# Kernel tuning notes

Hardware: AMD Instinct MI355X
Metric: run time of the kernel (lower is better)

## Reference

```python
import jax, jax.numpy as jnp
import numpy as np
from jax import lax

LN_EPS = 1e-6  # flax LayerNorm default


def _layernorm(x, scale, bias):
    mu = jnp.mean(x, axis=-1, keepdims=True)
    var = jnp.mean(jnp.square(x - mu), axis=-1, keepdims=True)
    return (x - mu) * lax.rsqrt(var + LN_EPS) * scale + bias


def _lstm_layer(c0, h0, Wi, Wh, b, x):
    # x: [B, T, F]; carry c/h: [B, H]; gate order i, f, g, o (flax)
    def step(carry, xt):
        c, h = carry
        z = xt @ Wi + h @ Wh + b  # [B, 4H]
        i, f, g, o = jnp.split(z, 4, axis=-1)
        i = jax.nn.sigmoid(i); f = jax.nn.sigmoid(f)
        g = jnp.tanh(g); o = jax.nn.sigmoid(o)
        c = f * c + i * g
        h = o * jnp.tanh(c)
        return (c, h), h
    (cT, hT), hs = lax.scan(step, (c0, h0), jnp.swapaxes(x, 0, 1))
    return cT, hT, jnp.swapaxes(hs, 0, 1)  # hs: [B, T, H]


def setup_inputs() -> dict:
    key = jax.random.key(0)
    ks = jax.random.split(key, 16)
    B, T, F, H, P, A = 64, 128, 512, 1024, 1024, 32
    s = 0.05
    return {
        "x": jax.random.normal(ks[0], (B, T, F), jnp.float32),
        "c0": jnp.zeros((2, B, H), jnp.float32),
        "h0": jnp.zeros((2, B, H), jnp.float32),
        "W_pre": jax.random.normal(ks[1], (F, P), jnp.float32) * s,
        "b_pre": jnp.zeros((P,), jnp.float32),
        "ln_scale": jnp.ones((P,), jnp.float32),
        "ln_bias": jnp.zeros((P,), jnp.float32),
        "Wi0": jax.random.normal(ks[2], (P, 4 * H), jnp.float32) * s,
        "Wh0": jax.random.normal(ks[3], (H, 4 * H), jnp.float32) * s,
        "b0": jnp.zeros((4 * H,), jnp.float32),
        "Wi1": jax.random.normal(ks[4], (H, 4 * H), jnp.float32) * s,
        "Wh1": jax.random.normal(ks[5], (H, 4 * H), jnp.float32) * s,
        "b1": jnp.zeros((4 * H,), jnp.float32),
        "W_post": jax.random.normal(ks[6], (H, P), jnp.float32) * s,
        "b_post": jnp.zeros((P,), jnp.float32),
        "W_out": jax.random.normal(ks[7], (P, A), jnp.float32) * s,
        "b_out": jnp.zeros((A,), jnp.float32),
        "training": False,
    }


def reference(x, c0, h0, W_pre, b_pre, ln_scale, ln_bias,
              Wi0, Wh0, b0, Wi1, Wh1, b1,
              W_post, b_post, W_out, b_out, training):
    # preprocessing: Dense -> LayerNorm -> relu
    h = jax.nn.relu(_layernorm(x @ W_pre + b_pre, ln_scale, ln_bias))
    # two stacked LSTM layers scanned over time
    c1, h1, h = _lstm_layer(c0[0], h0[0], Wi0, Wh0, b0, h)
    c2, h2, h = _lstm_layer(c0[1], h0[1], Wi1, Wh1, b1, h)
    # postprocessing: Dense -> relu (dropout deterministic => identity)
    h = jax.nn.relu(h @ W_post + b_post)
    logits = h @ W_out + b_out  # [B, T, action_dim]
    new_carry = (jnp.stack([c1, c2]), jnp.stack([h1, h2]))
    return new_carry, logits
```

## Files before the change

### kernel.cpp

```cpp
#include <hip/hip_runtime.h>
#include <hip/hip_bf16.h>
#include <math.h>

typedef __attribute__((ext_vector_type(8))) short short8;
typedef __attribute__((ext_vector_type(4))) float f32x4;
typedef __attribute__((ext_vector_type(4))) unsigned u32x4;
typedef unsigned short u16;
typedef unsigned long long u64;

__device__ __forceinline__ u16 f2bf(float f) {
    union { float f; unsigned u; } v; v.f = f;
    unsigned r = v.u + 0x7fffu + ((v.u >> 16) & 1u);
    return (u16)(r >> 16);
}
__device__ __forceinline__ float bf2f(u16 b) {
    union { unsigned u; float f; } v; v.u = ((unsigned)b) << 16;
    return v.f;
}
__device__ __forceinline__ float fast_sigmoid(float x) {
    return __builtin_amdgcn_rcpf(1.f + __expf(-x));
}
__device__ __forceinline__ float fast_tanh(float x) {
    return 1.f - 2.f * __builtin_amdgcn_rcpf(1.f + __expf(2.f * x));
}
__device__ __forceinline__ u32x4 ldg16(const void* p) {
    u32x4 r;
    asm volatile("global_load_dwordx4 %0, %1, off"
                 : "=v"(r) : "v"(p) : "memory");
    return r;
}


__global__ __launch_bounds__(256) void k_zero(unsigned* p, int n) {
    int i = blockIdx.x * 256 + threadIdx.x;
    if (i < n) p[i] = 0u;
}

__global__ __launch_bounds__(256) void k_cvt(const float* __restrict__ in,
                                             u16* __restrict__ out, int n) {
    int i = blockIdx.x * 256 + threadIdx.x;
    if (i < n) out[i] = f2bf(in[i]);
}

__global__ __launch_bounds__(256) void k_cvt_h(const float* __restrict__ in,
                                               u16* __restrict__ out) {
    int i = blockIdx.x * 256 + threadIdx.x;
    int b = i >> 10, j = i & 1023;
    out[(size_t)(j >> 3) * 512 + b * 8 + (j & 7)] = f2bf(in[i]);
}

__global__ __launch_bounds__(256) void k_transpose(const float* __restrict__ W,
                                                   u16* __restrict__ WT, int K, int N) {
    __shared__ float tile[32][33];
    int n0 = blockIdx.x * 32, k0 = blockIdx.y * 32;
    int tx = threadIdx.x & 31, ty = threadIdx.x >> 5;
    #pragma unroll
    for (int j = 0; j < 32; j += 8)
        tile[ty + j][tx] = W[(size_t)(k0 + ty + j) * N + n0 + tx];
    __syncthreads();
    #pragma unroll
    for (int j = 0; j < 32; j += 8)
        WT[(size_t)(n0 + ty + j) * K + k0 + tx] = f2bf(tile[tx][ty + j]);
}

template <int MODE>
__global__ __launch_bounds__(256) void k_gemm(const u16* __restrict__ A,
                                              const u16* __restrict__ BT,
                                              const float* __restrict__ bias,
                                              void* __restrict__ Cout,
                                              int M, int N, int K) {
    const int w = threadIdx.x >> 6, l = threadIdx.x & 63;
    const int lm = l & 15, lq = l >> 4;
    const int r0 = blockIdx.y * 64 + w * 16;
    const int c0 = blockIdx.x * 64;
    const u16* arow = A + (size_t)(r0 + lm) * K + lq * 8;
    const u16* bp0 = BT + (size_t)(c0 + lm) * K + lq * 8;
    const u16* bp1 = bp0 + (size_t)16 * K;
    const u16* bp2 = bp0 + (size_t)32 * K;
    const u16* bp3 = bp0 + (size_t)48 * K;
    f32x4 acc0 = {0.f, 0.f, 0.f, 0.f}, acc1 = acc0, acc2 = acc0, acc3 = acc0;
    for (int k0 = 0; k0 < K; k0 += 32) {
        short8 a = *(const short8*)(arow + k0);
        acc0 = __builtin_amdgcn_mfma_f32_16x16x32_bf16(a, *(const short8*)(bp0 + k0), acc0, 0, 0, 0);
        acc1 = __builtin_amdgcn_mfma_f32_16x16x32_bf16(a, *(const short8*)(bp1 + k0), acc1, 0, 0, 0);
        acc2 = __builtin_amdgcn_mfma_f32_16x16x32_bf16(a, *(const short8*)(bp2 + k0), acc2, 0, 0, 0);
        acc3 = __builtin_amdgcn_mfma_f32_16x16x32_bf16(a, *(const short8*)(bp3 + k0), acc3, 0, 0, 0);
    }
    f32x4 accs[4] = {acc0, acc1, acc2, acc3};
    #pragma unroll
    for (int nt = 0; nt < 4; nt++) {
        #pragma unroll
        for (int r = 0; r < 4; r++) {
            int row = r0 + lq * 4 + r;
            int col = c0 + nt * 16 + lm;
            float v = accs[nt][r] + bias[col];
            if (MODE == 0) {
                ((float*)Cout)[(size_t)row * N + col] = v;
            } else {
                if (MODE == 2) v = fmaxf(v, 0.f);
                ((u16*)Cout)[(size_t)row * N + col] = f2bf(v);
            }
        }
    }
}

__global__ __launch_bounds__(256) void k_ln_relu(const float* __restrict__ X,
                                                 const float* __restrict__ scale,
                                                 const float* __restrict__ bias,
                                                 u16* __restrict__ preS) {
    const int N = 1024;
    int row = blockIdx.x;
    int b = row >> 7, t = row & 127;
    const float* x = X + (size_t)row * N;
    __shared__ float vbuf[1024];
    float s = 0.f, ss = 0.f;
    float vals[4];
    #pragma unroll
    for (int j = 0; j < 4; j++) {
        float v = x[threadIdx.x + 256 * j];
        vals[j] = v; s += v; ss += v * v;
    }
    #pragma unroll
    for (int o = 32; o > 0; o >>= 1) { s += __shfl_down(s, o); ss += __shfl_down(ss, o); }
    __shared__ float rs[4], rss[4];
    int w = threadIdx.x >> 6;
    if ((threadIdx.x & 63) == 0) { rs[w] = s; rss[w] = ss; }
    __syncthreads();
    __shared__ float smu, sinv;
    if (threadIdx.x == 0) {
        float a = rs[0] + rs[1] + rs[2] + rs[3];
        float bq = rss[0] + rss[1] + rss[2] + rss[3];
        float mu = a * (1.f / N);
        float var = bq * (1.f / N) - mu * mu;
        smu = mu; sinv = rsqrtf(var + 1e-6f);
    }
    __syncthreads();
    float mu = smu, inv = sinv;
    #pragma unroll
    for (int j = 0; j < 4; j++) {
        int i = threadIdx.x + 256 * j;
        float v = (vals[j] - mu) * inv * scale[i] + bias[i];
        vbuf[i] = fmaxf(v, 0.f);
    }
    __syncthreads();
    if (threadIdx.x < 128) {
        int g = threadIdx.x;
        union { u16 h[8]; u32x4 v; } pk;
        #pragma unroll
        for (int e = 0; e < 8; e++) pk.h[e] = f2bf(vbuf[g * 8 + e]);
        *(u32x4*)(preS + (size_t)t * 65536 + (size_t)g * 512 + b * 8) = pk.v;
    }
}

#define FBLOCKS 256
__global__ __launch_bounds__(512, 1) void k_lstm_fused(
    const u16* __restrict__ WiT0, const u16* __restrict__ WhT0,
    const u16* __restrict__ WiT1, const u16* __restrict__ WhT1,
    const u16* __restrict__ preS, const float* __restrict__ b0v,
    const float* __restrict__ b1v, const float* __restrict__ c0_all,
    u16* __restrict__ hs0, u16* __restrict__ hs1, u16* __restrict__ Hp,
    float* __restrict__ out, unsigned* __restrict__ ctr) {
    const int bk = blockIdx.x;
    const int role = bk >> 7;
    const int bkl = bk & 127;
    const int tid = threadIdx.x;
    const int w = tid >> 6, l = tid & 63, lm = l & 15, lq = l >> 4;
    const int kp = w >> 2, rt = w & 3;

    __shared__ u16 whs[65536];
    __shared__ float zbuf[2 * 64 * 33];
    __shared__ int gflag[2];

    {
        const u16* Wx = role ? WiT1 : WiT0;
        const u16* Wh = role ? WhT1 : WhT0;
        for (int f = tid; f < 8192; f += 512) {
            int flm = f & 15, flq = (f >> 4) & 3;
            int fi = (f >> 6) & 31;
            int rest = f >> 11;
            int fg = rest & 1, fkp = (rest >> 1) & 1;
            int lc = fg * 16 + flm;
            int gcolw = (lc >> 3) * 1024 + bkl * 8 + (lc & 7);
            int k = fi * 32 + flq * 8;
            const u16* src = (fkp == 0 ? Wx : Wh) + (size_t)gcolw * 1024 + k;
            *(short8*)(whs + (size_t)f * 8) = *(const short8*)src;
        }
    }
    if (tid == 0) { gflag[0] = -1; gflag[1] = -1; }
    const int u = tid & 7, b = tid >> 3;
    const int gcol = bkl * 8 + u;
    float c = (c0_all + (size_t)role * 65536)[(size_t)b * 1024 + gcol];
    const float* bv = role ? b1v : b0v;
    float bi0 = bv[gcol], bi1 = bv[1024 + gcol];
    float bi2 = bv[2048 + gcol], bi3 = bv[3072 + gcol];
    u16* hs_my = role ? hs1 : hs0;
    float* c_out = out + (size_t)role * 65536;
    float* h_out = out + 131072 + (size_t)role * 65536;
    const int lanoff = (lq * 16 + lm) * 8;
    __syncthreads();

    for (int t = 0; t < 128; t++) {
        if (role || kp == 1) {
            int need = (role && kp == 0) ? t + 1 : t;
            if (rt == 0) {
                if (need > 0) {
                    int cbase = (role && kp) ? 128 : 0;
                    for (;;) {
                        unsigned a0 = __hip_atomic_load(&ctr[(cbase + l) * 16], __ATOMIC_RELAXED,
                                                        __HIP_MEMORY_SCOPE_AGENT);
                        unsigned a1 = __hip_atomic_load(&ctr[(cbase + 64 + l) * 16], __ATOMIC_RELAXED,
                                                        __HIP_MEMORY_SCOPE_AGENT);
                        if (__all((a0 >= (unsigned)need) && (a1 >= (unsigned)need))) break;
                        __builtin_amdgcn_s_sleep(1);
                    }
                }
                __hip_atomic_store(&gflag[kp], need, __ATOMIC_RELAXED,
                                   __HIP_MEMORY_SCOPE_WORKGROUP);
            } else {
                while (__hip_atomic_load(&gflag[kp], __ATOMIC_RELAXED,
                                         __HIP_MEMORY_SCOPE_WORKGROUP) < need)
                    __builtin_amdgcn_s_sleep(1);
            }
        }

        const u16* abase;
        if (!role) abase = (kp == 0) ? preS + (size_t)t * 65536
                                     : hs0 + (size_t)t * 65536;
        else       abase = (kp == 0) ? hs0 + (size_t)(t + 1) * 65536
                                     : hs1 + (size_t)t * 65536;
        const u16* arow = abase + (size_t)lq * 512 + (rt * 16 + lm) * 8;
        const u16* bw0 = whs + kp * 32768 + lanoff;

        f32x4 acc0 = {0.f, 0.f, 0.f, 0.f}, acc1 = acc0;
        #define STEPF(Ai, i)                                                      \
        {   union { u32x4 q; short8 v; } _a; _a.q = (Ai);                         \
            short8 _b0 = *(const short8*)(bw0 + (i) * 512);                       \
            short8 _b1 = *(const short8*)(bw0 + 16384 + (i) * 512);               \
            acc0 = __builtin_amdgcn_mfma_f32_16x16x32_bf16(_a.v, _b0, acc0, 0, 0, 0); \
            acc1 = __builtin_amdgcn_mfma_f32_16x16x32_bf16(_a.v, _b1, acc1, 0, 0, 0); }

        u32x4 A0 = ldg16(arow +     0), A1 = ldg16(arow +  2048);
        u32x4 A2 = ldg16(arow +  4096), A3 = ldg16(arow +  6144);
        u32x4 A4 = ldg16(arow +  8192), A5 = ldg16(arow + 10240);
        u32x4 A6 = ldg16(arow + 12288), A7 = ldg16(arow + 14336);
        u32x4 A8 = ldg16(arow + 16384), A9 = ldg16(arow + 18432);
        u32x4 A10 = ldg16(arow + 20480), A11 = ldg16(arow + 22528);
        u32x4 A12 = ldg16(arow + 24576), A13 = ldg16(arow + 26624);
        u32x4 A14 = ldg16(arow + 28672), A15 = ldg16(arow + 30720);
        u32x4 A16 = ldg16(arow + 32768), A17 = ldg16(arow + 34816);
        u32x4 A18 = ldg16(arow + 36864), A19 = ldg16(arow + 38912);
        u32x4 A20 = ldg16(arow + 40960), A21 = ldg16(arow + 43008);
        u32x4 A22 = ldg16(arow + 45056), A23 = ldg16(arow + 47104);
        u32x4 A24 = ldg16(arow + 49152), A25 = ldg16(arow + 51200);
        u32x4 A26 = ldg16(arow + 53248), A27 = ldg16(arow + 55296);
        u32x4 A28 = ldg16(arow + 57344), A29 = ldg16(arow + 59392);
        u32x4 A30 = ldg16(arow + 61440), A31 = ldg16(arow + 63488);
        asm volatile("s_waitcnt vmcnt(24)"
                     : "+v"(A0), "+v"(A1), "+v"(A2), "+v"(A3),
                       "+v"(A4), "+v"(A5), "+v"(A6), "+v"(A7) :: "memory");
        STEPF(A0, 0) STEPF(A1, 1) STEPF(A2, 2) STEPF(A3, 3)
        STEPF(A4, 4) STEPF(A5, 5) STEPF(A6, 6) STEPF(A7, 7)
        asm volatile("s_waitcnt vmcnt(16)"
                     : "+v"(A8), "+v"(A9), "+v"(A10), "+v"(A11),
                       "+v"(A12), "+v"(A13), "+v"(A14), "+v"(A15) :: "memory");
        STEPF(A8, 8) STEPF(A9, 9) STEPF(A10, 10) STEPF(A11, 11)
        STEPF(A12, 12) STEPF(A13, 13) STEPF(A14, 14) STEPF(A15, 15)
        asm volatile("s_waitcnt vmcnt(8)"
                     : "+v"(A16), "+v"(A17), "+v"(A18), "+v"(A19),
                       "+v"(A20), "+v"(A21), "+v"(A22), "+v"(A23) :: "memory");
        STEPF(A16, 16) STEPF(A17, 17) STEPF(A18, 18) STEPF(A19, 19)
        STEPF(A20, 20) STEPF(A21, 21) STEPF(A22, 22) STEPF(A23, 23)
        asm volatile("s_waitcnt vmcnt(0)"
                     : "+v"(A24), "+v"(A25), "+v"(A26), "+v"(A27),
                       "+v"(A28), "+v"(A29), "+v"(A30), "+v"(A31) :: "memory");
        STEPF(A24, 24) STEPF(A25, 25) STEPF(A26, 26) STEPF(A27, 27)
        STEPF(A28, 28) STEPF(A29, 29) STEPF(A30, 30) STEPF(A31, 31)
        #undef STEPF

        {
            float* zb = zbuf + (size_t)kp * 2112;
            #pragma unroll
            for (int r = 0; r < 4; r++) {
                int row = rt * 16 + lq * 4 + r;
                zb[row * 33 + lm] = acc0[r];
                zb[row * 33 + 16 + lm] = acc1[r];
            }
        }
        __syncthreads();

        {
            const float* z0 = zbuf + (size_t)b * 33;
            const float* z1 = z0 + 2112;
            float gi = z0[u]      + z1[u]      + bi0;
            float gf = z0[8 + u]  + z1[8 + u]  + bi1;
            float gg = z0[16 + u] + z1[16 + u] + bi2;
            float go = z0[24 + u] + z1[24 + u] + bi3;
            gi = fast_sigmoid(gi);
            gf = fast_sigmoid(gf);
            gg = fast_tanh(gg);
            go = fast_sigmoid(go);
            c = gf * c + gi * gg;
            float h = go * fast_tanh(c);
            unsigned hv = (unsigned)f2bf(h);
            int base = l & 56;
            unsigned p0 = __shfl(hv, base + 0, 64) | (__shfl(hv, base + 1, 64) << 16);
            unsigned p1 = __shfl(hv, base + 2, 64) | (__shfl(hv, base + 3, 64) << 16);
            unsigned p2 = __shfl(hv, base + 4, 64) | (__shfl(hv, base + 5, 64) << 16);
            unsigned p3 = __shfl(hv, base + 6, 64) | (__shfl(hv, base + 7, 64) << 16);
            if (u == 0) {
                u32x4 pv = {p0, p1, p2, p3};
                u16* dst = hs_my + (size_t)(t + 1) * 65536 + (size_t)bkl * 512 + b * 8;
                asm volatile("global_store_dwordx4 %0, %1, off sc0 sc1"
                             :: "v"(dst), "v"(pv) : "memory");
                if (role) {
                    u16* d2 = Hp + (size_t)(t * 64 + b) * 1024 + bkl * 8;
                    *(u32x4*)d2 = pv;
                }
            }
            if (t == 127) {
                c_out[(size_t)b * 1024 + gcol] = c;
                h_out[(size_t)b * 1024 + gcol] = h;
            }
        }
        __syncthreads();

        if (tid == 0)
            __hip_atomic_store(&ctr[bk * 16], (unsigned)(t + 1), __ATOMIC_RELAXED,
                               __HIP_MEMORY_SCOPE_AGENT);
    }
}

__global__ __launch_bounds__(256) void k_logits(const u16* __restrict__ Pact,
                                                const u16* __restrict__ WoT,
                                                const float* __restrict__ bout,
                                                float* __restrict__ out) {
    int r = blockIdx.x * 8 + (threadIdx.x >> 5);
    int n = threadIdx.x & 31;
    const u16* a = Pact + (size_t)r * 1024;
    const u16* wv = WoT + (size_t)n * 1024;
    float s = 0.f;
    for (int k = 0; k < 1024; k += 8) {
        short8 av = *(const short8*)(a + k);
        short8 wvv = *(const short8*)(wv + k);
        #pragma unroll
        for (int j = 0; j < 8; j++)
            s += bf2f((u16)av[j]) * bf2f((u16)wvv[j]);
    }
    int t = r >> 6, b = r & 63;
    out[((size_t)b * 128 + t) * 32 + n] = s + bout[n];
}

extern "C" void kernel_launch(void* const* d_in, const int* in_sizes, int n_in,
                              void* d_out, int out_size, void* d_ws, size_t ws_size,
                              hipStream_t stream) {
    const float* x      = (const float*)d_in[0];
    const float* c0     = (const float*)d_in[1];
    const float* h0     = (const float*)d_in[2];
    const float* W_pre  = (const float*)d_in[3];
    const float* b_pre  = (const float*)d_in[4];
    const float* ln_s   = (const float*)d_in[5];
    const float* ln_b   = (const float*)d_in[6];
    const float* Wi0    = (const float*)d_in[7];
    const float* Wh0    = (const float*)d_in[8];
    const float* b0     = (const float*)d_in[9];
    const float* Wi1    = (const float*)d_in[10];
    const float* Wh1    = (const float*)d_in[11];
    const float* b1     = (const float*)d_in[12];
    const float* W_post = (const float*)d_in[13];
    const float* b_post = (const float*)d_in[14];
    const float* W_out  = (const float*)d_in[15];
    const float* b_out  = (const float*)d_in[16];
    float* out = (float*)d_out;

    char* ws = (char*)d_ws;
    size_t off = 0;
    auto alloc = [&](size_t bytes) {
        void* p = ws + off;
        off += (bytes + 255) & ~(size_t)255;
        return p;
    };
    u16* WTpre  = (u16*)alloc((size_t)1024 * 512 * 2);
    u16* WTi0   = (u16*)alloc((size_t)4096 * 1024 * 2);
    u16* WTh0   = (u16*)alloc((size_t)4096 * 1024 * 2);
    u16* WTi1   = (u16*)alloc((size_t)4096 * 1024 * 2);
    u16* WTh1   = (u16*)alloc((size_t)4096 * 1024 * 2);
    u16* WTpost = (u16*)alloc((size_t)1024 * 1024 * 2);
    u16* WTout  = (u16*)alloc((size_t)32 * 1024 * 2);
    u16* Xb     = (u16*)alloc((size_t)8192 * 512 * 2);
    u16* preS   = (u16*)alloc((size_t)128 * 65536 * 2);
    u16* hs0    = (u16*)alloc((size_t)129 * 65536 * 2);
    u16* hs1    = (u16*)alloc((size_t)129 * 65536 * 2);
    u16* postact= (u16*)alloc((size_t)8192 * 1024 * 2);
    unsigned* ctr = (unsigned*)alloc(32768);
    void* unionreg = alloc((size_t)8192 * 4096 * 2);
    float* pre_f32 = (float*)unionreg;
    u16* Hplain = (u16*)unionreg;

    k_zero<<<32, 256, 0, stream>>>(ctr, 8192);
    k_cvt<<<(8192 * 512) / 256, 256, 0, stream>>>(x, Xb, 8192 * 512);
    k_cvt_h<<<256, 256, 0, stream>>>(h0, hs0);
    k_cvt_h<<<256, 256, 0, stream>>>(h0 + 65536, hs1);

    k_transpose<<<dim3(32, 16), 256, 0, stream>>>(W_pre, WTpre, 512, 1024);
    k_transpose<<<dim3(128, 32), 256, 0, stream>>>(Wi0, WTi0, 1024, 4096);
    k_transpose<<<dim3(128, 32), 256, 0, stream>>>(Wh0, WTh0, 1024, 4096);
    k_transpose<<<dim3(128, 32), 256, 0, stream>>>(Wi1, WTi1, 1024, 4096);
    k_transpose<<<dim3(128, 32), 256, 0, stream>>>(Wh1, WTh1, 1024, 4096);
    k_transpose<<<dim3(32, 32), 256, 0, stream>>>(W_post, WTpost, 1024, 1024);
    k_transpose<<<dim3(1, 32), 256, 0, stream>>>(W_out, WTout, 1024, 32);

    k_gemm<0><<<dim3(16, 128), 256, 0, stream>>>(Xb, WTpre, b_pre, pre_f32, 8192, 1024, 512);
    k_ln_relu<<<8192, 256, 0, stream>>>(pre_f32, ln_s, ln_b, preS);

    {
        const u16* WiT0_ = WTi0; const u16* WhT0_ = WTh0;
        const u16* WiT1_ = WTi1; const u16* WhT1_ = WTh1;
        const u16* preS_ = preS; const float* b0_ = b0; const float* b1_ = b1;
        const float* c0_ = c0; u16* hs0_ = hs0; u16* hs1_ = hs1;
        u16* Hp_ = Hplain; float* out_ = out; unsigned* ctr_ = ctr;
        void* args[] = {&WiT0_, &WhT0_, &WiT1_, &WhT1_, &preS_, &b0_, &b1_,
                        &c0_, &hs0_, &hs1_, &Hp_, &out_, &ctr_};
        hipLaunchCooperativeKernel((void*)k_lstm_fused, dim3(FBLOCKS), dim3(512),
                                   args, 0, stream);
    }

    k_gemm<2><<<dim3(16, 128), 256, 0, stream>>>(Hplain, WTpost, b_post, postact,
                                                 8192, 1024, 1024);
    k_logits<<<1024, 256, 0, stream>>>(postact, WTout, b_out, out + 262144);
}
```

Baseline: 1.154 ms.

## Replace layer-0 recurrent counter barrier with sentinel-polled data readiness

For the layer-0 recurrent half, the per-step wait on global atomic counters from all 128 blocks is replaced by polling the hidden-state data itself. A shadow buffer is pre-filled with a NaN bf16 sentinel, each block writes its new h there, and readers spin until the loaded values no longer match the sentinel. This lets each wave start its MFMA groups as soon as its own slice arrives, removing a counter round-trip and the workgroup flag handoff. The cost is an extra store per step, a fill kernel, and extra cache-bypassing reloads. It also assumes a real hidden value can never equal the sentinel pattern.

```diff
diff --git a/kernel.cpp b/kernel.cpp
--- a/kernel.cpp
+++ b/kernel.cpp
@@ -29,11 +29,23 @@
                  : "=v"(r) : "v"(p) : "memory");
     return r;
 }
+__device__ __forceinline__ u32x4 ldg16sc(const void* p) {
+    u32x4 r;
+    asm volatile("global_load_dwordx4 %0, %1, off sc0 sc1"
+                 : "=v"(r) : "v"(p) : "memory");
+    return r;
+}
 
 
 __global__ __launch_bounds__(256) void k_zero(unsigned* p, int n) {
     int i = blockIdx.x * 256 + threadIdx.x;
     if (i < n) p[i] = 0u;
+}
+
+__global__ __launch_bounds__(256) void k_fill_sent(u32x4* p, int n) {
+    int i = blockIdx.x * 256 + threadIdx.x;
+    u32x4 s = {0x7F807F80u, 0x7F807F80u, 0x7F807F80u, 0x7F807F80u};
+    if (i < n) p[i] = s;
 }
 
 __global__ __launch_bounds__(256) void k_cvt(const float* __restrict__ in,
@@ -158,8 +170,8 @@
     const u16* __restrict__ WiT1, const u16* __restrict__ WhT1,
     const u16* __restrict__ preS, const float* __restrict__ b0v,
     const float* __restrict__ b1v, const float* __restrict__ c0_all,
-    u16* __restrict__ hs0, u16* __restrict__ hs1, u16* __restrict__ Hp,
-    float* __restrict__ out, unsigned* __restrict__ ctr) {
+    u16* __restrict__ hs0, u16* __restrict__ hs1, u16* __restrict__ hsS,
+    u16* __restrict__ Hp, float* __restrict__ out, unsigned* __restrict__ ctr) {
     const int bk = blockIdx.x;
     const int role = bk >> 7;
     const int bkl = bk & 127;
@@ -200,38 +212,9 @@
     __syncthreads();
 
     for (int t = 0; t < 128; t++) {
-        if (role || kp == 1) {
-            int need = (role && kp == 0) ? t + 1 : t;
-            if (rt == 0) {
-                if (need > 0) {
-                    int cbase = (role && kp) ? 128 : 0;
-                    for (;;) {
-                        unsigned a0 = __hip_atomic_load(&ctr[(cbase + l) * 16], __ATOMIC_RELAXED,
-                                                        __HIP_MEMORY_SCOPE_AGENT);
-                        unsigned a1 = __hip_atomic_load(&ctr[(cbase + 64 + l) * 16], __ATOMIC_RELAXED,
-                                                        __HIP_MEMORY_SCOPE_AGENT);
-                        if (__all((a0 >= (unsigned)need) && (a1 >= (unsigned)need))) break;
-                        __builtin_amdgcn_s_sleep(1);
-                    }
-                }
-                __hip_atomic_store(&gflag[kp], need, __ATOMIC_RELAXED,
-                                   __HIP_MEMORY_SCOPE_WORKGROUP);
-            } else {
-                while (__hip_atomic_load(&gflag[kp], __ATOMIC_RELAXED,
-                                         __HIP_MEMORY_SCOPE_WORKGROUP) < need)
-                    __builtin_amdgcn_s_sleep(1);
-            }
-        }
-
-        const u16* abase;
-        if (!role) abase = (kp == 0) ? preS + (size_t)t * 65536
-                                     : hs0 + (size_t)t * 65536;
-        else       abase = (kp == 0) ? hs0 + (size_t)(t + 1) * 65536
-                                     : hs1 + (size_t)t * 65536;
-        const u16* arow = abase + (size_t)lq * 512 + (rt * 16 + lm) * 8;
         const u16* bw0 = whs + kp * 32768 + lanoff;
-
         f32x4 acc0 = {0.f, 0.f, 0.f, 0.f}, acc1 = acc0;
+
         #define STEPF(Ai, i)                                                      \
         {   union { u32x4 q; short8 v; } _a; _a.q = (Ai);                         \
             short8 _b0 = *(const short8*)(bw0 + (i) * 512);                       \
@@ -239,42 +222,134 @@
             acc0 = __builtin_amdgcn_mfma_f32_16x16x32_bf16(_a.v, _b0, acc0, 0, 0, 0); \
             acc1 = __builtin_amdgcn_mfma_f32_16x16x32_bf16(_a.v, _b1, acc1, 0, 0, 0); }
 
-        u32x4 A0 = ldg16(arow +     0), A1 = ldg16(arow +  2048);
-        u32x4 A2 = ldg16(arow +  4096), A3 = ldg16(arow +  6144);
-        u32x4 A4 = ldg16(arow +  8192), A5 = ldg16(arow + 10240);
-        u32x4 A6 = ldg16(arow + 12288), A7 = ldg16(arow + 14336);
-        u32x4 A8 = ldg16(arow + 16384), A9 = ldg16(arow + 18432);
-        u32x4 A10 = ldg16(arow + 20480), A11 = ldg16(arow + 22528);
-        u32x4 A12 = ldg16(arow + 24576), A13 = ldg16(arow + 26624);
-        u32x4 A14 = ldg16(arow + 28672), A15 = ldg16(arow + 30720);
-        u32x4 A16 = ldg16(arow + 32768), A17 = ldg16(arow + 34816);
-        u32x4 A18 = ldg16(arow + 36864), A19 = ldg16(arow + 38912);
-        u32x4 A20 = ldg16(arow + 40960), A21 = ldg16(arow + 43008);
-        u32x4 A22 = ldg16(arow + 45056), A23 = ldg16(arow + 47104);
-        u32x4 A24 = ldg16(arow + 49152), A25 = ldg16(arow + 51200);
-        u32x4 A26 = ldg16(arow + 53248), A27 = ldg16(arow + 55296);
-        u32x4 A28 = ldg16(arow + 57344), A29 = ldg16(arow + 59392);
-        u32x4 A30 = ldg16(arow + 61440), A31 = ldg16(arow + 63488);
-        asm volatile("s_waitcnt vmcnt(24)"
-                     : "+v"(A0), "+v"(A1), "+v"(A2), "+v"(A3),
-                       "+v"(A4), "+v"(A5), "+v"(A6), "+v"(A7) :: "memory");
-        STEPF(A0, 0) STEPF(A1, 1) STEPF(A2, 2) STEPF(A3, 3)
-        STEPF(A4, 4) STEPF(A5, 5) STEPF(A6, 6) STEPF(A7, 7)
-        asm volatile("s_waitcnt vmcnt(16)"
-                     : "+v"(A8), "+v"(A9), "+v"(A10), "+v"(A11),
-                       "+v"(A12), "+v"(A13), "+v"(A14), "+v"(A15) :: "memory");
-        STEPF(A8, 8) STEPF(A9, 9) STEPF(A10, 10) STEPF(A11, 11)
-        STEPF(A12, 12) STEPF(A13, 13) STEPF(A14, 14) STEPF(A15, 15)
-        asm volatile("s_waitcnt vmcnt(8)"
-                     : "+v"(A16), "+v"(A17), "+v"(A18), "+v"(A19),
-                       "+v"(A20), "+v"(A21), "+v"(A22), "+v"(A23) :: "memory");
-        STEPF(A16, 16) STEPF(A17, 17) STEPF(A18, 18) STEPF(A19, 19)
-        STEPF(A20, 20) STEPF(A21, 21) STEPF(A22, 22) STEPF(A23, 23)
-        asm volatile("s_waitcnt vmcnt(0)"
-                     : "+v"(A24), "+v"(A25), "+v"(A26), "+v"(A27),
-                       "+v"(A28), "+v"(A29), "+v"(A30), "+v"(A31) :: "memory");
-        STEPF(A24, 24) STEPF(A25, 25) STEPF(A26, 26) STEPF(A27, 27)
-        STEPF(A28, 28) STEPF(A29, 29) STEPF(A30, 30) STEPF(A31, 31)
+        if (!role && kp == 1) {
+            const u16* arow = hsS + (size_t)t * 65536 + lq * 512 + (rt * 16 + lm) * 8;
+            #define CHK4(q) (((q)[0] != 0x7F807F80u) && ((q)[1] != 0x7F807F80u) && \
+                             ((q)[2] != 0x7F807F80u) && ((q)[3] != 0x7F807F80u))
+            #define SGROUP(B0,B1,B2,B3,B4,B5,B6,B7,o0,o1,o2,o3,o4,o5,o6,o7)       \
+            for (;;) {                                                            \
+                int _ok = CHK4(B0) && CHK4(B1) && CHK4(B2) && CHK4(B3) &&         \
+                          CHK4(B4) && CHK4(B5) && CHK4(B6) && CHK4(B7);           \
+                if (__all(_ok)) break;                                            \
+                B0 = ldg16sc(arow + o0); B1 = ldg16sc(arow + o1);                 \
+                B2 = ldg16sc(arow + o2); B3 = ldg16sc(arow + o3);                 \
+                B4 = ldg16sc(arow + o4); B5 = ldg16sc(arow + o5);                 \
+                B6 = ldg16sc(arow + o6); B7 = ldg16sc(arow + o7);                 \
+                asm volatile("s_waitcnt vmcnt(0)"                                 \
+                             : "+v"(B0), "+v"(B1), "+v"(B2), "+v"(B3),            \
+                               "+v"(B4), "+v"(B5), "+v"(B6), "+v"(B7) :: "memory"); \
+            }
+            u32x4 A0 = ldg16sc(arow +     0), A1 = ldg16sc(arow +  2048);
+            u32x4 A2 = ldg16sc(arow +  4096), A3 = ldg16sc(arow +  6144);
+            u32x4 A4 = ldg16sc(arow +  8192), A5 = ldg16sc(arow + 10240);
+            u32x4 A6 = ldg16sc(arow + 12288), A7 = ldg16sc(arow + 14336);
+            u32x4 A8 = ldg16sc(arow + 16384), A9 = ldg16sc(arow + 18432);
+            u32x4 A10 = ldg16sc(arow + 20480), A11 = ldg16sc(arow + 22528);
+            u32x4 A12 = ldg16sc(arow + 24576), A13 = ldg16sc(arow + 26624);
+            u32x4 A14 = ldg16sc(arow + 28672), A15 = ldg16sc(arow + 30720);
+            u32x4 A16 = ldg16sc(arow + 32768), A17 = ldg16sc(arow + 34816);
+            u32x4 A18 = ldg16sc(arow + 36864), A19 = ldg16sc(arow + 38912);
+            u32x4 A20 = ldg16sc(arow + 40960), A21 = ldg16sc(arow + 43008);
+            u32x4 A22 = ldg16sc(arow + 45056), A23 = ldg16sc(arow + 47104);
+            u32x4 A24 = ldg16sc(arow + 49152), A25 = ldg16sc(arow + 51200);
+            u32x4 A26 = ldg16sc(arow + 53248), A27 = ldg16sc(arow + 55296);
+            u32x4 A28 = ldg16sc(arow + 57344), A29 = ldg16sc(arow + 59392);
+            u32x4 A30 = ldg16sc(arow + 61440), A31 = ldg16sc(arow + 63488);
+            asm volatile("s_waitcnt vmcnt(24)"
+                         : "+v"(A0), "+v"(A1), "+v"(A2), "+v"(A3),
+                           "+v"(A4), "+v"(A5), "+v"(A6), "+v"(A7) :: "memory");
+            SGROUP(A0,A1,A2,A3,A4,A5,A6,A7, 0,2048,4096,6144,8192,10240,12288,14336)
+            STEPF(A0, 0) STEPF(A1, 1) STEPF(A2, 2) STEPF(A3, 3)
+            STEPF(A4, 4) STEPF(A5, 5) STEPF(A6, 6) STEPF(A7, 7)
+            asm volatile("s_waitcnt vmcnt(16)"
+                         : "+v"(A8), "+v"(A9), "+v"(A10), "+v"(A11),
+                           "+v"(A12), "+v"(A13), "+v"(A14), "+v"(A15) :: "memory");
+            SGROUP(A8,A9,A10,A11,A12,A13,A14,A15,
+                   16384,18432,20480,22528,24576,26624,28672,30720)
+            STEPF(A8, 8) STEPF(A9, 9) STEPF(A10, 10) STEPF(A11, 11)
+            STEPF(A12, 12) STEPF(A13, 13) STEPF(A14, 14) STEPF(A15, 15)
+            asm volatile("s_waitcnt vmcnt(8)"
+                         : "+v"(A16), "+v"(A17), "+v"(A18), "+v"(A19),
+                           "+v"(A20), "+v"(A21), "+v"(A22), "+v"(A23) :: "memory");
+            SGROUP(A16,A17,A18,A19,A20,A21,A22,A23,
+                   32768,34816,36864,38912,40960,43008,45056,47104)
+            STEPF(A16, 16) STEPF(A17, 17) STEPF(A18, 18) STEPF(A19, 19)
+            STEPF(A20, 20) STEPF(A21, 21) STEPF(A22, 22) STEPF(A23, 23)
+            asm volatile("s_waitcnt vmcnt(0)"
+                         : "+v"(A24), "+v"(A25), "+v"(A26), "+v"(A27),
+                           "+v"(A28), "+v"(A29), "+v"(A30), "+v"(A31) :: "memory");
+            SGROUP(A24,A25,A26,A27,A28,A29,A30,A31,
+                   49152,51200,53248,55296,57344,59392,61440,63488)
+            STEPF(A24, 24) STEPF(A25, 25) STEPF(A26, 26) STEPF(A27, 27)
+            STEPF(A28, 28) STEPF(A29, 29) STEPF(A30, 30) STEPF(A31, 31)
+            #undef SGROUP
+            #undef CHK4
+        } else {
+            if (role) {
+                int need = (kp == 0) ? t + 1 : t;
+                if (rt == 0) {
+                    if (need > 0) {
+                        int cbase = kp ? 128 : 0;
+                        for (;;) {
+                            unsigned a0 = __hip_atomic_load(&ctr[(cbase + l) * 16], __ATOMIC_RELAXED,
+                                                            __HIP_MEMORY_SCOPE_AGENT);
+                            unsigned a1 = __hip_atomic_load(&ctr[(cbase + 64 + l) * 16], __ATOMIC_RELAXED,
+                                                            __HIP_MEMORY_SCOPE_AGENT);
+                            if (__all((a0 >= (unsigned)need) && (a1 >= (unsigned)need))) break;
+                            __builtin_amdgcn_s_sleep(1);
+                        }
+                    }
+                    __hip_atomic_store(&gflag[kp], need, __ATOMIC_RELAXED,
+                                       __HIP_MEMORY_SCOPE_WORKGROUP);
+                } else {
+                    while (__hip_atomic_load(&gflag[kp], __ATOMIC_RELAXED,
+                                             __HIP_MEMORY_SCOPE_WORKGROUP) < need)
+                        __builtin_amdgcn_s_sleep(1);
+                }
+            }
+            const u16* abase;
+            if (!role) abase = preS + (size_t)t * 65536;
+            else       abase = (kp == 0) ? hs0 + (size_t)(t + 1) * 65536
+                                         : hs1 + (size_t)t * 65536;
+            const u16* arow = abase + (size_t)lq * 512 + (rt * 16 + lm) * 8;
+
+            u32x4 A0 = ldg16(arow +     0), A1 = ldg16(arow +  2048);
+            u32x4 A2 = ldg16(arow +  4096), A3 = ldg16(arow +  6144);
+            u32x4 A4 = ldg16(arow +  8192), A5 = ldg16(arow + 10240);
+            u32x4 A6 = ldg16(arow + 12288), A7 = ldg16(arow + 14336);
+            u32x4 A8 = ldg16(arow + 16384), A9 = ldg16(arow + 18432);
+            u32x4 A10 = ldg16(arow + 20480), A11 = ldg16(arow + 22528);
+            u32x4 A12 = ldg16(arow + 24576), A13 = ldg16(arow + 26624);
+            u32x4 A14 = ldg16(arow + 28672), A15 = ldg16(arow + 30720);
+            u32x4 A16 = ldg16(arow + 32768), A17 = ldg16(arow + 34816);
+            u32x4 A18 = ldg16(arow + 36864), A19 = ldg16(arow + 38912);
+            u32x4 A20 = ldg16(arow + 40960), A21 = ldg16(arow + 43008);
+            u32x4 A22 = ldg16(arow + 45056), A23 = ldg16(arow + 47104);
+            u32x4 A24 = ldg16(arow + 49152), A25 = ldg16(arow + 51200);
+            u32x4 A26 = ldg16(arow + 53248), A27 = ldg16(arow + 55296);
+            u32x4 A28 = ldg16(arow + 57344), A29 = ldg16(arow + 59392);
+            u32x4 A30 = ldg16(arow + 61440), A31 = ldg16(arow + 63488);
+            asm volatile("s_waitcnt vmcnt(24)"
+                         : "+v"(A0), "+v"(A1), "+v"(A2), "+v"(A3),
+                           "+v"(A4), "+v"(A5), "+v"(A6), "+v"(A7) :: "memory");
+            STEPF(A0, 0) STEPF(A1, 1) STEPF(A2, 2) STEPF(A3, 3)
+            STEPF(A4, 4) STEPF(A5, 5) STEPF(A6, 6) STEPF(A7, 7)
+            asm volatile("s_waitcnt vmcnt(16)"
+                         : "+v"(A8), "+v"(A9), "+v"(A10), "+v"(A11),
+                           "+v"(A12), "+v"(A13), "+v"(A14), "+v"(A15) :: "memory");
+            STEPF(A8, 8) STEPF(A9, 9) STEPF(A10, 10) STEPF(A11, 11)
+            STEPF(A12, 12) STEPF(A13, 13) STEPF(A14, 14) STEPF(A15, 15)
+            asm volatile("s_waitcnt vmcnt(8)"
+                         : "+v"(A16), "+v"(A17), "+v"(A18), "+v"(A19),
+                           "+v"(A20), "+v"(A21), "+v"(A22), "+v"(A23) :: "memory");
+            STEPF(A16, 16) STEPF(A17, 17) STEPF(A18, 18) STEPF(A19, 19)
+            STEPF(A20, 20) STEPF(A21, 21) STEPF(A22, 22) STEPF(A23, 23)
+            asm volatile("s_waitcnt vmcnt(0)"
+                         : "+v"(A24), "+v"(A25), "+v"(A26), "+v"(A27),
+                           "+v"(A28), "+v"(A29), "+v"(A30), "+v"(A31) :: "memory");
+            STEPF(A24, 24) STEPF(A25, 25) STEPF(A26, 26) STEPF(A27, 27)
+            STEPF(A28, 28) STEPF(A29, 29) STEPF(A30, 30) STEPF(A31, 31)
+        }
         #undef STEPF
 
         {
@@ -312,7 +387,11 @@
                 u16* dst = hs_my + (size_t)(t + 1) * 65536 + (size_t)bkl * 512 + b * 8;
                 asm volatile("global_store_dwordx4 %0, %1, off sc0 sc1"
                              :: "v"(dst), "v"(pv) : "memory");
-                if (role) {
+                if (!role) {
+                    u16* d3 = hsS + (size_t)(t + 1) * 65536 + (size_t)bkl * 512 + b * 8;
+                    asm volatile("global_store_dwordx4 %0, %1, off sc0 sc1"
+                                 :: "v"(d3), "v"(pv) : "memory");
+                } else {
                     u16* d2 = Hp + (size_t)(t * 64 + b) * 1024 + bkl * 8;
                     *(u32x4*)d2 = pv;
                 }
@@ -390,6 +469,7 @@
     u16* preS   = (u16*)alloc((size_t)128 * 65536 * 2);
     u16* hs0    = (u16*)alloc((size_t)129 * 65536 * 2);
     u16* hs1    = (u16*)alloc((size_t)129 * 65536 * 2);
+    u16* hsS    = (u16*)alloc((size_t)129 * 65536 * 2);
     u16* postact= (u16*)alloc((size_t)8192 * 1024 * 2);
     unsigned* ctr = (unsigned*)alloc(32768);
     void* unionreg = alloc((size_t)8192 * 4096 * 2);
@@ -397,8 +477,10 @@
     u16* Hplain = (u16*)unionreg;
 
     k_zero<<<32, 256, 0, stream>>>(ctr, 8192);
+    k_fill_sent<<<4096, 256, 0, stream>>>((u32x4*)(hsS + 65536), 1048576);
     k_cvt<<<(8192 * 512) / 256, 256, 0, stream>>>(x, Xb, 8192 * 512);
     k_cvt_h<<<256, 256, 0, stream>>>(h0, hs0);
+    k_cvt_h<<<256, 256, 0, stream>>>(h0, hsS);
     k_cvt_h<<<256, 256, 0, stream>>>(h0 + 65536, hs1);
 
     k_transpose<<<dim3(32, 16), 256, 0, stream>>>(W_pre, WTpre, 512, 1024);
@@ -416,10 +498,10 @@
         const u16* WiT0_ = WTi0; const u16* WhT0_ = WTh0;
         const u16* WiT1_ = WTi1; const u16* WhT1_ = WTh1;
         const u16* preS_ = preS; const float* b0_ = b0; const float* b1_ = b1;
-        const float* c0_ = c0; u16* hs0_ = hs0; u16* hs1_ = hs1;
+        const float* c0_ = c0; u16* hs0_ = hs0; u16* hs1_ = hs1; u16* hsS_ = hsS;
         u16* Hp_ = Hplain; float* out_ = out; unsigned* ctr_ = ctr;
         void* args[] = {&WiT0_, &WhT0_, &WiT1_, &WhT1_, &preS_, &b0_, &b1_,
-                        &c0_, &hs0_, &hs1_, &Hp_, &out_, &ctr_};
+                        &c0_, &hs0_, &hs1_, &hsS_, &Hp_, &out_, &ctr_};
         hipLaunchCooperativeKernel((void*)k_lstm_fused, dim3(FBLOCKS), dim3(512),
                                    args, 0, stream);
     }
```

After: 1.299 ms. 1.13x slower.

## Merge prep kernels, poll counters per wave, split MFMA accumulator chains

Applied to the files above, without the earlier changes.

Eleven small preprocessing launches (zeroing, bf16 conversion, weight transposes) are merged into one k_prep kernel that dispatches on block index, cutting launch overhead. In the cooperative LSTM kernel, every wave now polls the global step counters itself instead of one wave polling and relaying through a shared-memory flag. The counters are packed contiguously rather than padded 16 apart. Each MFMA accumulator is split into four independent chains that are summed at the end, to shorten the dependency chain per time step. The trade-offs are more global polling traffic from all waves and possible false sharing on the packed counters.

```diff
diff --git a/kernel.cpp b/kernel.cpp
--- a/kernel.cpp
+++ b/kernel.cpp
@@ -30,30 +30,13 @@
     return r;
 }
 
-
-__global__ __launch_bounds__(256) void k_zero(unsigned* p, int n) {
-    int i = blockIdx.x * 256 + threadIdx.x;
-    if (i < n) p[i] = 0u;
-}
-
-__global__ __launch_bounds__(256) void k_cvt(const float* __restrict__ in,
-                                             u16* __restrict__ out, int n) {
-    int i = blockIdx.x * 256 + threadIdx.x;
-    if (i < n) out[i] = f2bf(in[i]);
-}
-
-__global__ __launch_bounds__(256) void k_cvt_h(const float* __restrict__ in,
-                                               u16* __restrict__ out) {
-    int i = blockIdx.x * 256 + threadIdx.x;
-    int b = i >> 10, j = i & 1023;
-    out[(size_t)(j >> 3) * 512 + b * 8 + (j & 7)] = f2bf(in[i]);
-}
-
-__global__ __launch_bounds__(256) void k_transpose(const float* __restrict__ W,
-                                                   u16* __restrict__ WT, int K, int N) {
-    __shared__ float tile[32][33];
-    int n0 = blockIdx.x * 32, k0 = blockIdx.y * 32;
-    int tx = threadIdx.x & 31, ty = threadIdx.x >> 5;
+__device__ __forceinline__ void tr_tile(const float* __restrict__ W,
+                                        u16* __restrict__ WT, int K, int N,
+                                        int bid, int tid, float (*tile)[33]) {
+    int gx = N >> 5;
+    int bx = bid % gx, by = bid / gx;
+    int n0 = bx * 32, k0 = by * 32;
+    int tx = tid & 31, ty = tid >> 5;
     #pragma unroll
     for (int j = 0; j < 32; j += 8)
         tile[ty + j][tx] = W[(size_t)(k0 + ty + j) * N + n0 + tx];
@@ -62,6 +45,53 @@
     for (int j = 0; j < 32; j += 8)
         WT[(size_t)(n0 + ty + j) * K + k0 + tx] = f2bf(tile[tx][ty + j]);
 }
+
+__global__ __launch_bounds__(256) void k_prep(
+    const float* __restrict__ x, u16* __restrict__ Xb,
+    const float* __restrict__ h0, u16* __restrict__ hs0, u16* __restrict__ hs1,
+    unsigned* __restrict__ ctr,
+    const float* __restrict__ Wpre, u16* __restrict__ WTpre,
+    const float* __restrict__ Wi0, u16* __restrict__ WTi0,
+    const float* __restrict__ Wh0, u16* __restrict__ WTh0,
+    const float* __restrict__ Wi1, u16* __restrict__ WTi1,
+    const float* __restrict__ Wh1, u16* __restrict__ WTh1,
+    const float* __restrict__ Wpost, u16* __restrict__ WTpost,
+    const float* __restrict__ Wout, u16* __restrict__ WTout) {
+    __shared__ float tile[32][33];
+    int bid = blockIdx.x, tid = threadIdx.x;
+    if (bid == 0) { ctr[tid] = 0u; return; }
+    bid -= 1;
+    if (bid < 16384) {
+        int i = bid * 256 + tid;
+        Xb[i] = f2bf(x[i]);
+        return;
+    }
+    bid -= 16384;
+    if (bid < 512) {
+        int i = bid * 256 + tid;
+        int layer = i >> 16, j = i & 65535;
+        int b = j >> 10, jj = j & 1023;
+        u16 v = f2bf(h0[(size_t)layer * 65536 + j]);
+        u16* dst = layer ? hs1 : hs0;
+        dst[(size_t)(jj >> 3) * 512 + b * 8 + (jj & 7)] = v;
+        return;
+    }
+    bid -= 512;
+    if (bid < 512)  { tr_tile(Wpre,  WTpre,  512,  1024, bid, tid, tile); return; }
+    bid -= 512;
+    if (bid < 4096) { tr_tile(Wi0,   WTi0,   1024, 4096, bid, tid, tile); return; }
+    bid -= 4096;
+    if (bid < 4096) { tr_tile(Wh0,   WTh0,   1024, 4096, bid, tid, tile); return; }
+    bid -= 4096;
+    if (bid < 4096) { tr_tile(Wi1,   WTi1,   1024, 4096, bid, tid, tile); return; }
+    bid -= 4096;
+    if (bid < 4096) { tr_tile(Wh1,   WTh1,   1024, 4096, bid, tid, tile); return; }
+    bid -= 4096;
+    if (bid < 1024) { tr_tile(Wpost, WTpost, 1024, 1024, bid, tid, tile); return; }
+    bid -= 1024;
+    tr_tile(Wout, WTout, 1024, 32, bid, tid, tile);
+}
+#define PREP_BLOCKS (1 + 16384 + 512 + 512 + 4 * 4096 + 1024 + 32)
 
 template <int MODE>
 __global__ __launch_bounds__(256) void k_gemm(const u16* __restrict__ A,
@@ -169,7 +199,6 @@
 
     __shared__ u16 whs[65536];
     __shared__ float zbuf[2 * 64 * 33];
-    __shared__ int gflag[2];
 
     {
         const u16* Wx = role ? WiT1 : WiT0;
@@ -186,7 +215,6 @@
             *(short8*)(whs + (size_t)f * 8) = *(const short8*)src;
         }
     }
-    if (tid == 0) { gflag[0] = -1; gflag[1] = -1; }
     const int u = tid & 7, b = tid >> 3;
     const int gcol = bkl * 8 + u;
     float c = (c0_all + (size_t)role * 65536)[(size_t)b * 1024 + gcol];
@@ -200,26 +228,19 @@
     __syncthreads();
 
     for (int t = 0; t < 128; t++) {
-        if (role || kp == 1) {
-            int need = (role && kp == 0) ? t + 1 : t;
-            if (rt == 0) {
-                if (need > 0) {
-                    int cbase = (role && kp) ? 128 : 0;
-                    for (;;) {
-                        unsigned a0 = __hip_atomic_load(&ctr[(cbase + l) * 16], __ATOMIC_RELAXED,
-                                                        __HIP_MEMORY_SCOPE_AGENT);
-                        unsigned a1 = __hip_atomic_load(&ctr[(cbase + 64 + l) * 16], __ATOMIC_RELAXED,
-                                                        __HIP_MEMORY_SCOPE_AGENT);
-                        if (__all((a0 >= (unsigned)need) && (a1 >= (unsigned)need))) break;
-                        __builtin_amdgcn_s_sleep(1);
-                    }
+        {
+            int need, base;
+            if (!role) { need = (kp == 1) ? t : 0;     base = 0; }
+            else       { need = (kp == 0) ? t + 1 : t; base = (kp == 0) ? 0 : 128; }
+            if (need > 0) {
+                for (;;) {
+                    unsigned a0 = __hip_atomic_load(&ctr[base + l], __ATOMIC_RELAXED,
+                                                    __HIP_MEMORY_SCOPE_AGENT);
+                    unsigned a1 = __hip_atomic_load(&ctr[base + 64 + l], __ATOMIC_RELAXED,
+                                                    __HIP_MEMORY_SCOPE_AGENT);
+                    if (__all((a0 >= (unsigned)need) && (a1 >= (unsigned)need))) break;
+                    __builtin_amdgcn_s_sleep(1);
                 }
-                __hip_atomic_store(&gflag[kp], need, __ATOMIC_RELAXED,
-                                   __HIP_MEMORY_SCOPE_WORKGROUP);
-            } else {
-                while (__hip_atomic_load(&gflag[kp], __ATOMIC_RELAXED,
-                                         __HIP_MEMORY_SCOPE_WORKGROUP) < need)
-                    __builtin_amdgcn_s_sleep(1);
             }
         }
 
@@ -231,13 +252,14 @@
         const u16* arow = abase + (size_t)lq * 512 + (rt * 16 + lm) * 8;
         const u16* bw0 = whs + kp * 32768 + lanoff;
 
-        f32x4 acc0 = {0.f, 0.f, 0.f, 0.f}, acc1 = acc0;
+        f32x4 zv = {0.f, 0.f, 0.f, 0.f};
+        f32x4 ac0[4] = {zv, zv, zv, zv}, ac1[4] = {zv, zv, zv, zv};
         #define STEPF(Ai, i)                                                      \
         {   union { u32x4 q; short8 v; } _a; _a.q = (Ai);                         \
             short8 _b0 = *(const short8*)(bw0 + (i) * 512);                       \
             short8 _b1 = *(const short8*)(bw0 + 16384 + (i) * 512);               \
-            acc0 = __builtin_amdgcn_mfma_f32_16x16x32_bf16(_a.v, _b0, acc0, 0, 0, 0); \
-            acc1 = __builtin_amdgcn_mfma_f32_16x16x32_bf16(_a.v, _b1, acc1, 0, 0, 0); }
+            ac0[(i) & 3] = __builtin_amdgcn_mfma_f32_16x16x32_bf16(_a.v, _b0, ac0[(i) & 3], 0, 0, 0); \
+            ac1[(i) & 3] = __builtin_amdgcn_mfma_f32_16x16x32_bf16(_a.v, _b1, ac1[(i) & 3], 0, 0, 0); }
 
         u32x4 A0 = ldg16(arow +     0), A1 = ldg16(arow +  2048);
         u32x4 A2 = ldg16(arow +  4096), A3 = ldg16(arow +  6144);
@@ -276,6 +298,8 @@
         STEPF(A24, 24) STEPF(A25, 25) STEPF(A26, 26) STEPF(A27, 27)
         STEPF(A28, 28) STEPF(A29, 29) STEPF(A30, 30) STEPF(A31, 31)
         #undef STEPF
+        f32x4 acc0 = (ac0[0] + ac0[1]) + (ac0[2] + ac0[3]);
+        f32x4 acc1 = (ac1[0] + ac1[1]) + (ac1[2] + ac1[3]);
 
         {
             float* zb = zbuf + (size_t)kp * 2112;
@@ -325,7 +349,7 @@
         __syncthreads();
 
         if (tid == 0)
-            __hip_atomic_store(&ctr[bk * 16], (unsigned)(t + 1), __ATOMIC_RELAXED,
+            __hip_atomic_store(&ctr[bk], (unsigned)(t + 1), __ATOMIC_RELAXED,
                                __HIP_MEMORY_SCOPE_AGENT);
     }
 }
@@ -396,18 +420,10 @@
     float* pre_f32 = (float*)unionreg;
     u16* Hplain = (u16*)unionreg;
 
-    k_zero<<<32, 256, 0, stream>>>(ctr, 8192);
-    k_cvt<<<(8192 * 512) / 256, 256, 0, stream>>>(x, Xb, 8192 * 512);
-    k_cvt_h<<<256, 256, 0, stream>>>(h0, hs0);
-    k_cvt_h<<<256, 256, 0, stream>>>(h0 + 65536, hs1);
-
-    k_transpose<<<dim3(32, 16), 256, 0, stream>>>(W_pre, WTpre, 512, 1024);
-    k_transpose<<<dim3(128, 32), 256, 0, stream>>>(Wi0, WTi0, 1024, 4096);
-    k_transpose<<<dim3(128, 32), 256, 0, stream>>>(Wh0, WTh0, 1024, 4096);
-    k_transpose<<<dim3(128, 32), 256, 0, stream>>>(Wi1, WTi1, 1024, 4096);
-    k_transpose<<<dim3(128, 32), 256, 0, stream>>>(Wh1, WTh1, 1024, 4096);
-    k_transpose<<<dim3(32, 32), 256, 0, stream>>>(W_post, WTpost, 1024, 1024);
-    k_transpose<<<dim3(1, 32), 256, 0, stream>>>(W_out, WTout, 1024, 32);
+    k_prep<<<PREP_BLOCKS, 256, 0, stream>>>(
+        x, Xb, h0, hs0, hs1, ctr,
+        W_pre, WTpre, Wi0, WTi0, Wh0, WTh0, Wi1, WTi1, Wh1, WTh1,
+        W_post, WTpost, W_out, WTout);
 
     k_gemm<0><<<dim3(16, 128), 256, 0, stream>>>(Xb, WTpre, b_pre, pre_f32, 8192, 1024, 512);
     k_ln_relu<<<8192, 256, 0, stream>>>(pre_f32, ln_s, ln_b, preS);
```

New measurement: 1.442 ms. 24.9% more time.
